# Kernel tuning notes

Hardware: AMD Instinct MI355X
Metric: run time of the kernel (lower is better)

The kernel has to match this reference:

```python
import jax, jax.numpy as jnp
import numpy as np

N_HIDDEN = 512

def _lstm_cell(x, h, c, W_ih, W_hh, b):
    # PyTorch LSTMCell: gates ordered i, f, g, o
    gates = x @ W_ih.T + h @ W_hh.T + b  # [B, 4H]
    i, f, g, o = jnp.split(gates, 4, axis=-1)
    i = jax.nn.sigmoid(i)
    f = jax.nn.sigmoid(f)
    g = jnp.tanh(g)
    o = jax.nn.sigmoid(o)
    c_new = f * c + i * g
    h_new = o * jnp.tanh(c_new)
    return h_new, c_new

def setup_inputs() -> dict:
    key = jax.random.key(0)
    ks = jax.random.split(key, 10)
    B, T, H = 256, 1024, N_HIDDEN
    s1 = 1.0 / np.sqrt(H)
    inp = {
        'x': jax.random.normal(ks[0], (B, T), dtype=jnp.float32),
        'W_ih1': jax.random.uniform(ks[1], (4 * H, 1), jnp.float32, -s1, s1),
        'W_hh1': jax.random.uniform(ks[2], (4 * H, H), jnp.float32, -s1, s1),
        'b1': jax.random.uniform(ks[3], (4 * H,), jnp.float32, -s1, s1),
        'W_ih2': jax.random.uniform(ks[4], (4 * H, H), jnp.float32, -s1, s1),
        'W_hh2': jax.random.uniform(ks[5], (4 * H, H), jnp.float32, -s1, s1),
        'b2': jax.random.uniform(ks[6], (4 * H,), jnp.float32, -s1, s1),
        'W_lin': jax.random.uniform(ks[7], (1, H), jnp.float32, -s1, s1),
        'b_lin': jax.random.uniform(ks[8], (1,), jnp.float32, -s1, s1),
    }
    return inp

def reference(x, W_ih1, W_hh1, b1, W_ih2, W_hh2, b2, W_lin, b_lin):
    B, T = x.shape
    H = W_hh1.shape[1]
    zeros = jnp.zeros((B, H), dtype=x.dtype)
    init = (zeros, zeros, zeros, zeros)
    xs = x.T[:, :, None]  # [T, B, 1]

    def step(carry, x_t):
        h1, c1, h2, c2 = carry
        h1, c1 = _lstm_cell(x_t, h1, c1, W_ih1, W_hh1, b1)
        h2, c2 = _lstm_cell(h1, h2, c2, W_ih2, W_hh2, b2)
        out = h2 @ W_lin.T + b_lin  # [B, 1]
        return (h1, c1, h2, c2), out

    _, outs = jax.lax.scan(step, init, xs)  # outs: [T, B, 1]
    return outs[:, :, 0].T  # [B, T]
```

## Files before the change

### kernel.cpp

```cpp
#include <hip/hip_runtime.h>
#include <math.h>

#define BB   256
#define TT   1024
#define HH   512
#define NWG  256
#define NTHR 512
#define SLOT (HH*BB)
#define NSLOT 8
#define PADX 20

typedef _Float16 f16;
typedef _Float16 f16x8 __attribute__((ext_vector_type(8)));
typedef float    f32x4 __attribute__((ext_vector_type(4)));
typedef unsigned int u32;
typedef u32 u32x2 __attribute__((ext_vector_type(2)));
typedef u32 u32x4 __attribute__((ext_vector_type(4)));
typedef unsigned short u16;
typedef unsigned char u8;

__device__ __forceinline__ f32x4 mf(f16x8 a, f16x8 b, f32x4 c){
  return __builtin_amdgcn_mfma_f32_16x16x32_f16(a, b, c, 0, 0, 0);
}

__device__ __forceinline__ float fast_sigmoid(float v){
  float e = __expf(-v);
  return __builtin_amdgcn_rcpf(1.0f + e);
}
__device__ __forceinline__ float fast_tanh(float v){
  float a = fabsf(v);
  float e = __expf(-2.0f * a);
  float r = (1.0f - e) * __builtin_amdgcn_rcpf(1.0f + e);
  return copysignf(r, v);
}

__device__ __forceinline__ void split_h(float hv, u16& hb, u8& lb){
  const f16 hh = (f16)hv;
  const f16 lh = (f16)((hv - (float)hh) * 2048.0f);
  union {f16 f; u16 u;} ch, cl; ch.f = hh; cl.f = lh;
  hb = ch.u;
  lb = (u8)(((u32)cl.u + 0x80u) >> 8);
}
__device__ __forceinline__ float join_h(u16 hb, u8 lb){
  union {u16 u; f16 f;} h, l;
  h.u = hb; l.u = (u16)((u32)lb << 8);
  return (float)h.f + (float)l.f * (1.0f/2048.0f);
}
__device__ __forceinline__ void st_wt_u16(u16* p, u16 v){
  __hip_atomic_store(p, v, __ATOMIC_RELAXED, __HIP_MEMORY_SCOPE_AGENT);
}
__device__ __forceinline__ void st_wt_u8(u8* p, u8 v){
  __hip_atomic_store(p, v, __ATOMIC_RELAXED, __HIP_MEMORY_SCOPE_AGENT);
}
__device__ __forceinline__ void st_wt_f32(float* p, float v){
  __hip_atomic_store(p, v, __ATOMIC_RELAXED, __HIP_MEMORY_SCOPE_AGENT);
}

__device__ __forceinline__ void build2(u32x4 hd, u32x2 ld2, f16x8& fh, f16x8& fl){
  union {u32 u[4]; f16x8 f;} H, L;
  H.u[0]=hd[0]; H.u[1]=hd[1]; H.u[2]=hd[2]; H.u[3]=hd[3];
  L.u[0] = __builtin_amdgcn_perm(ld2[0], 0u, 0x05010400u);
  L.u[1] = __builtin_amdgcn_perm(ld2[0], 0u, 0x07010600u);
  L.u[2] = __builtin_amdgcn_perm(ld2[1], 0u, 0x05010400u);
  L.u[3] = __builtin_amdgcn_perm(ld2[1], 0u, 0x07010600u);
  fh = H.f; fl = L.f;
}

struct St1 { u32x4 h4; u32x2 l2; };

__device__ __forceinline__ void gridbar_g(unsigned* barb, unsigned ph){
  __syncthreads();
  if (threadIdx.x == 0){
    __builtin_amdgcn_fence(__ATOMIC_RELEASE, "agent");
    const unsigned g = blockIdx.x & 31u;
    unsigned old = __hip_atomic_fetch_add(&barb[g*16], 1u, __ATOMIC_RELAXED, __HIP_MEMORY_SCOPE_AGENT);
    if (old + 1u == 8u*ph){
      unsigned om = __hip_atomic_fetch_add(&barb[512], 1u, __ATOMIC_RELAXED, __HIP_MEMORY_SCOPE_AGENT);
      if (om + 1u == 32u*ph){
        #pragma unroll
        for (int r = 0; r < 32; ++r)
          __hip_atomic_store(&barb[544 + r*16], ph, __ATOMIC_RELAXED, __HIP_MEMORY_SCOPE_AGENT);
      }
    }
    while (__hip_atomic_load(&barb[544 + g*16], __ATOMIC_RELAXED, __HIP_MEMORY_SCOPE_AGENT) < ph){
      __builtin_amdgcn_s_sleep(2);
    }
    __builtin_amdgcn_fence(__ATOMIC_ACQUIRE, "agent");
  }
  __syncthreads();
}

__global__ __launch_bounds__(NTHR, 2) void lstm_mfma(
    const float* __restrict__ x,      const float* __restrict__ W_ih1,
    const float* __restrict__ W_hh1,  const float* __restrict__ b1,
    const float* __restrict__ W_ih2,  const float* __restrict__ W_hh2,
    const float* __restrict__ b2,     const float* __restrict__ W_lin,
    const float* __restrict__ b_lin,  float* __restrict__ out,
    char* __restrict__ wsb)
{
  __shared__ f16x8 A2hi[2048], A2lo[2048], A1hi[1024], A1lo[1024];
  __shared__ float xch[8][16*PADX];
  __shared__ float wlin_s[512];
  __shared__ float outpart[2][8];

  unsigned* bar = (unsigned*)wsb;
  float* xT = (float*)(wsb + 16384);
  u16* h1h = (u16*)(wsb + 16384 + 1048576);
  u8*  h1l = (u8*) ((char*)h1h + 2*NSLOT*SLOT);
  u16* h2h = (u16*)((char*)h1l + NSLOT*SLOT);
  u8*  h2l = (u8*) ((char*)h2h + 2*NSLOT*SLOT);

  const int w   = blockIdx.x,  tid = threadIdx.x;
  const int l   = tid & 63,    wv  = tid >> 6;
  const int quad = l >> 4,     lc  = l & 15;
  const int p = w >> 1, cb = w & 1;
  const int j0 = 4*p;
  const int bcol = cb*128 + wv*16 + lc;
  const int jq = j0 + quad;
  const int b_out = cb*128 + p;
  unsigned* dbar = bar + cb*1024;
  unsigned* gbar = bar + 2048;
  const unsigned grp = (unsigned)(p >> 3);
  const int qrot = p & 3;
  const int hoff = (p>>1)*2048 + bcol*8 + (p&1)*4 + quad;

  {
    const int g_ = lc >> 2, jj_ = lc & 3;
    const int wrow = g_*HH + j0 + jj_;
    const float* rowI  = W_ih2 + (size_t)wrow*HH;
    const float* rowH2 = W_hh2 + (size_t)wrow*HH;
    const float* rowH1 = W_hh1 + (size_t)wrow*HH;
    for (int c = wv; c < 32; c += 8){
      const int kb = c*32 + quad*8;
      union {f16x8 v; f16 e[8];} hi8, lo8;
      #pragma unroll
      for (int i = 0; i < 8; ++i){
        const int k = kb + i;
        const float wval = (k < HH) ? rowI[k] : rowH2[k - HH];
        const f16 h_ = (f16)wval;
        hi8.e[i] = h_;
        lo8.e[i] = (f16)((wval - (float)h_) * 2048.0f);
      }
      A2hi[c*64 + l] = hi8.v;
      A2lo[c*64 + l] = lo8.v;
    }
    for (int c = wv; c < 16; c += 8){
      const int kb = c*32 + quad*8;
      union {f16x8 v; f16 e[8];} hi8, lo8;
      #pragma unroll
      for (int i = 0; i < 8; ++i){
        const float wval = rowH1[kb + i];
        const f16 h_ = (f16)wval;
        hi8.e[i] = h_;
        lo8.e[i] = (f16)((wval - (float)h_) * 2048.0f);
      }
      A1hi[c*64 + l] = hi8.v;
      A1lo[c*64 + l] = lo8.v;
    }
  }
  float wih1r[4], b1r[4], b2r[4];
  #pragma unroll
  for (int g = 0; g < 4; ++g){
    wih1r[g] = W_ih1[g*HH + jq];
    b1r[g]   = b1[g*HH + jq];
    b2r[g]   = b2[g*HH + jq];
  }
  const float blin = b_lin[0];
  wlin_s[tid] = W_lin[tid];

  {
    const int gid = w*NTHR + tid;
    #pragma unroll
    for (int i2 = 0; i2 < 2; ++i2){
      const int idx = gid + i2*131072;
      const int bb2 = idx >> 10, tt2 = idx & (TT-1);
      xT[(size_t)tt2*BB + bb2] = x[idx];
    }
  }
  {
    const int idx = w*NTHR + tid;
    st_wt_u16(&h2h[(NSLOT-1)*SLOT + idx], (u16)0);
    st_wt_u8 (&h2l[(NSLOT-1)*SLOT + idx], (u8)0);
  }

  gridbar_g(gbar, 1);

  float c1, c2 = 0.0f;
  {
    const float xv0 = xT[bcol];
    const float gi = fast_sigmoid(fmaf(xv0, wih1r[0], b1r[0]));
    const float gg = fast_tanh   (fmaf(xv0, wih1r[2], b1r[2]));
    const float go = fast_sigmoid(fmaf(xv0, wih1r[3], b1r[3]));
    c1 = gi * gg;
    const float hv = go * fast_tanh(c1);
    u16 hb; u8 lb; split_h(hv, hb, lb);
    st_wt_u16(&h1h[hoff], hb);
    st_wt_u8 (&h1l[hoff], lb);
  }
  gridbar_g(gbar, 2);

  auto poll2 = [&](unsigned need) -> unsigned {
    const int li = l & 31;
    const unsigned off = (unsigned)((li & 15) * 16) + ((li & 16) ? 576u : 0u);
    unsigned cv = __hip_atomic_load(&dbar[off], __ATOMIC_RELAXED, __HIP_MEMORY_SCOPE_AGENT);
    return (unsigned)__ballot(cv >= need);
  };

  unsigned got = 0xFFFFFFFFu;

  for (int t = 0; t < TT; ++t){
    const int sR1 = ( t            & (NSLOT-1))*SLOT;
    const int sR2 = ((t+NSLOT-1)   & (NSLOT-1))*SLOT;
    const int sW1 = ((t+1)         & (NSLOT-1))*SLOT;
    const int sW2 = ( t            & (NSLOT-1))*SLOT;
    const unsigned need = 8u * (unsigned)t;

    f32x4 aA2 = {0,0,0,0}, aB2 = {0,0,0,0}, aA1 = {0,0,0,0}, aB1 = {0,0,0,0};
    const u16* q1h = h1h + sR1 + quad*2048 + bcol*8;
    const u8*  q1l = h1l + sR1 + quad*2048 + bcol*8;
    const u16* q2h = h2h + sR2 + quad*2048 + bcol*8;
    const u8*  q2l = h2l + sR2 + quad*2048 + bcol*8;

    auto waitq = [&](int qq, int base){
      const unsigned qm = 0xFu << (base + 4*qq);
      while ((got & qm) != qm){
        __builtin_amdgcn_s_sleep(1);
        got |= poll2(need);
      }
      asm volatile("" ::: "memory");
    };
    auto ldc1 = [&](int c) -> St1 {
      St1 s; s.h4 = *(const u32x4*)(q1h + c*8192); s.l2 = *(const u32x2*)(q1l + c*8192); return s;
    };
    auto ldc2 = [&](int c) -> St1 {
      St1 s; s.h4 = *(const u32x4*)(q2h + c*8192); s.l2 = *(const u32x2*)(q2l + c*8192); return s;
    };
    auto cmp1 = [&](const St1& s, int c){
      f16x8 bh, bl;
      build2(s.h4, s.l2, bh, bl);
      const f16x8 a2h = A2hi[c*64 + l];
      const f16x8 a2l = A2lo[c*64 + l];
      const f16x8 a1h = A1hi[c*64 + l];
      const f16x8 a1l = A1lo[c*64 + l];
      aA2 = mf(a2h, bh, aA2);
      aB2 = mf(a2h, bl, aB2);
      aB2 = mf(a2l, bh, aB2);
      aA1 = mf(a1h, bh, aA1);
      aB1 = mf(a1h, bl, aB1);
      aB1 = mf(a1l, bh, aB1);
    };
    auto cmp2 = [&](const St1& s, int c){
      f16x8 ch, cl2;
      build2(s.h4, s.l2, ch, cl2);
      const f16x8 d2h = A2hi[(c+16)*64 + l];
      const f16x8 d2l = A2lo[(c+16)*64 + l];
      aA2 = mf(d2h, ch, aA2);
      aB2 = mf(d2h, cl2, aB2);
      aB2 = mf(d2l, ch, aB2);
    };

    const int cq0 = 4*qrot;
    const int cq1 = 4*((qrot+1)&3);
    const int cq2 = 4*((qrot+2)&3);
    const int cq3 = 4*((qrot+3)&3);

    {
      St1 SA0,SA1,SA2,SA3, SB0,SB1,SB2,SB3;
      waitq(cq0 >> 2, 16);
      SA0=ldc1(cq0+0); SA1=ldc1(cq0+1); SA2=ldc1(cq0+2); SA3=ldc1(cq0+3);
      waitq(cq1 >> 2, 16);
      SB0=ldc1(cq1+0); SB1=ldc1(cq1+1); SB2=ldc1(cq1+2); SB3=ldc1(cq1+3);
      cmp1(SA0,cq0+0); cmp1(SA1,cq0+1); cmp1(SA2,cq0+2); cmp1(SA3,cq0+3);
      waitq(cq2 >> 2, 16);
      SA0=ldc1(cq2+0); SA1=ldc1(cq2+1); SA2=ldc1(cq2+2); SA3=ldc1(cq2+3);
      cmp1(SB0,cq1+0); cmp1(SB1,cq1+1); cmp1(SB2,cq1+2); cmp1(SB3,cq1+3);
      waitq(cq3 >> 2, 16);
      SB0=ldc1(cq3+0); SB1=ldc1(cq3+1); SB2=ldc1(cq3+2); SB3=ldc1(cq3+3);
      cmp1(SA0,cq2+0); cmp1(SA1,cq2+1); cmp1(SA2,cq2+2); cmp1(SA3,cq2+3);
      cmp1(SB0,cq3+0); cmp1(SB1,cq3+1); cmp1(SB2,cq3+2); cmp1(SB3,cq3+3);
    }

    float* xw = &xch[wv][0];
    {
      f32x4 pre;
      #pragma unroll
      for (int i = 0; i < 4; ++i) pre[i] = fmaf(aB1[i], 1.0f/2048.0f, aA1[i]);
      __threadfence_block();
      *(f32x4*)&xw[lc*PADX + quad*4] = pre;
      __threadfence_block();
      const float g0 = xw[lc*PADX + 0*4 + quad];
      const float g1 = xw[lc*PADX + 1*4 + quad];
      const float g2 = xw[lc*PADX + 2*4 + quad];
      const float g3 = xw[lc*PADX + 3*4 + quad];
      const int tx = (t+1 < TT) ? (t+1) : (TT-1);
      const float xv = xT[(size_t)tx*BB + bcol];
      const float gi = fast_sigmoid(g0 + fmaf(xv, wih1r[0], b1r[0]));
      const float gf = fast_sigmoid(g1 + fmaf(xv, wih1r[1], b1r[1]));
      const float gg = fast_tanh   (g2 + fmaf(xv, wih1r[2], b1r[2]));
      const float go = fast_sigmoid(g3 + fmaf(xv, wih1r[3], b1r[3]));
      c1 = fmaf(gf, c1, gi*gg);
      const float hv = go * fast_tanh(c1);
      u16 hb; u8 lb; split_h(hv, hb, lb);
      st_wt_u16(&h1h[sW1 + hoff], hb);
      st_wt_u8 (&h1l[sW1 + hoff], lb);
    }
    __syncthreads();
    if (tid == 0){
      __builtin_amdgcn_fence(__ATOMIC_RELEASE, "workgroup");
      __hip_atomic_fetch_add(&dbar[576 + grp*16], 1u, __ATOMIC_RELAXED, __HIP_MEMORY_SCOPE_AGENT);
    }

    u16 ohb; u8 olb;
    {
      St1 SA0,SA1,SA2,SA3, SB0,SB1,SB2,SB3;
      waitq(cq0 >> 2, 0);
      SA0=ldc2(cq0+0); SA1=ldc2(cq0+1); SA2=ldc2(cq0+2); SA3=ldc2(cq0+3);
      waitq(cq1 >> 2, 0);
      SB0=ldc2(cq1+0); SB1=ldc2(cq1+1); SB2=ldc2(cq1+2); SB3=ldc2(cq1+3);
      cmp2(SA0,cq0+0); cmp2(SA1,cq0+1); cmp2(SA2,cq0+2); cmp2(SA3,cq0+3);
      waitq(cq2 >> 2, 0);
      SA0=ldc2(cq2+0); SA1=ldc2(cq2+1); SA2=ldc2(cq2+2); SA3=ldc2(cq2+3);
      cmp2(SB0,cq1+0); cmp2(SB1,cq1+1); cmp2(SB2,cq1+2); cmp2(SB3,cq1+3);
      waitq(cq3 >> 2, 0);
      SB0=ldc2(cq3+0); SB1=ldc2(cq3+1); SB2=ldc2(cq3+2); SB3=ldc2(cq3+3);
      const int oidx = sR2 + (tid>>3)*2048 + b_out*8 + (tid&7);
      ohb = h2h[oidx];
      olb = h2l[oidx];
      cmp2(SA0,cq2+0); cmp2(SA1,cq2+1); cmp2(SA2,cq2+2); cmp2(SA3,cq2+3);
      cmp2(SB0,cq3+0); cmp2(SB1,cq3+1); cmp2(SB2,cq3+2); cmp2(SB3,cq3+3);
    }

    float opart = join_h(ohb, olb) * wlin_s[tid];

    {
      f32x4 pre;
      #pragma unroll
      for (int i = 0; i < 4; ++i) pre[i] = fmaf(aB2[i], 1.0f/2048.0f, aA2[i]);
      __threadfence_block();
      *(f32x4*)&xw[lc*PADX + quad*4] = pre;
      __threadfence_block();
      const float g0 = xw[lc*PADX + 0*4 + quad];
      const float g1 = xw[lc*PADX + 1*4 + quad];
      const float g2 = xw[lc*PADX + 2*4 + quad];
      const float g3 = xw[lc*PADX + 3*4 + quad];
      const float gi = fast_sigmoid(g0 + b2r[0]);
      const float gf = fast_sigmoid(g1 + b2r[1]);
      const float gg = fast_tanh   (g2 + b2r[2]);
      const float go = fast_sigmoid(g3 + b2r[3]);
      c2 = fmaf(gf, c2, gi*gg);
      const float hv = go * fast_tanh(c2);
      u16 hb; u8 lb; split_h(hv, hb, lb);
      st_wt_u16(&h2h[sW2 + hoff], hb);
      st_wt_u8 (&h2l[sW2 + hoff], lb);
    }
    #pragma unroll
    for (int off = 32; off > 0; off >>= 1) opart += __shfl_down(opart, off, 64);
    if (l == 0) outpart[t & 1][wv] = opart;

    __syncthreads();
    if (tid == 0){
      __builtin_amdgcn_fence(__ATOMIC_RELEASE, "workgroup");
      __hip_atomic_fetch_add(&dbar[grp*16], 1u, __ATOMIC_RELAXED, __HIP_MEMORY_SCOPE_AGENT);
      if (t % 7 == 6){
        __builtin_amdgcn_fence(__ATOMIC_ACQUIRE, "agent");
      }
      if (t > 0){
        float s = blin;
        #pragma unroll
        for (int q2i = 0; q2i < 8; ++q2i) s += outpart[t & 1][q2i];
        st_wt_f32(&out[(size_t)b_out*TT + (t-1)], s);
      }
    }
    got = poll2(8u * (unsigned)(t+1));
    __syncthreads();
  }

  {
    const unsigned needT = 8u * (unsigned)TT;
    while ((got & 0xFFFFu) != 0xFFFFu){
      __builtin_amdgcn_s_sleep(1);
      got |= poll2(needT);
    }
    asm volatile("" ::: "memory");

    const int oidx = ((TT-1)&(NSLOT-1))*SLOT + (tid>>3)*2048 + b_out*8 + (tid&7);
    float opart = join_h(h2h[oidx], h2l[oidx]) * wlin_s[tid];
    #pragma unroll
    for (int off = 32; off > 0; off >>= 1) opart += __shfl_down(opart, off, 64);
    if (l == 0) outpart[0][wv] = opart;
    __syncthreads();
    if (tid == 0){
      float s = blin;
      #pragma unroll
      for (int q2i = 0; q2i < 8; ++q2i) s += outpart[0][q2i];
      st_wt_f32(&out[(size_t)b_out*TT + (TT-1)], s);
    }
  }
}

extern "C" void kernel_launch(void* const* d_in, const int* in_sizes, int n_in,
                              void* d_out, int out_size, void* d_ws, size_t ws_size,
                              hipStream_t stream) {
  const float* x     = (const float*)d_in[0];
  const float* W_ih1 = (const float*)d_in[1];
  const float* W_hh1 = (const float*)d_in[2];
  const float* b1    = (const float*)d_in[3];
  const float* W_ih2 = (const float*)d_in[4];
  const float* W_hh2 = (const float*)d_in[5];
  const float* b2    = (const float*)d_in[6];
  const float* W_lin = (const float*)d_in[7];
  const float* b_lin = (const float*)d_in[8];
  float* out = (float*)d_out;
  char* wsb  = (char*)d_ws;

  hipMemsetAsync(d_ws, 0, 16384, stream);

  hipLaunchKernelGGL(lstm_mfma, dim3(NWG), dim3(NTHR), 0, stream,
                     x, W_ih1, W_hh1, b1, W_ih2, W_hh2, b2, W_lin, b_lin, out, wsb);
}
```

Measured before the change: 13.03 ms.

## Move layer-2 input matmul after layer-1 publish and swap barrier roles

Layer-1's phase now computes only the W_hh1 product, issuing all 16 chunk loads before any MFMA. The W_ih2·h1 product moves into layer-2's phase, where both h1 and h2 chunks are loaded together. The two dbar counters swap roles so each phase waits on the right producer. The output reduction moves to a different thread and the trailing __syncthreads is dropped, aiming to publish h1 sooner and shorten the critical path between workgroups. The trade-offs are more register pressure from holding all 16 chunks, a heavier layer-2 phase, and subtle risks to ordering and correctness from the changed synchronisation.

```diff
diff --git a/kernel.cpp b/kernel.cpp
--- a/kernel.cpp
+++ b/kernel.cpp
@@ -66,6 +66,7 @@
   fh = H.f; fl = L.f;
 }
 
+struct St  { u32x4 h1h4; u32x2 h1l2; u32x4 h2h4; u32x2 h2l2; };
 struct St1 { u32x4 h4; u32x2 l2; };
 
 __device__ __forceinline__ void gridbar_g(unsigned* barb, unsigned ph){
@@ -215,7 +216,6 @@
     const int sW2 = ( t            & (NSLOT-1))*SLOT;
     const unsigned need = 8u * (unsigned)t;
 
-    f32x4 aA2 = {0,0,0,0}, aB2 = {0,0,0,0}, aA1 = {0,0,0,0}, aB1 = {0,0,0,0};
     const u16* q1h = h1h + sR1 + quad*2048 + bcol*8;
     const u8*  q1l = h1l + sR1 + quad*2048 + bcol*8;
     const u16* q2h = h2h + sR2 + quad*2048 + bcol*8;
@@ -229,55 +229,39 @@
       }
       asm volatile("" ::: "memory");
     };
-    auto ldc1 = [&](int c) -> St1 {
-      St1 s; s.h4 = *(const u32x4*)(q1h + c*8192); s.l2 = *(const u32x2*)(q1l + c*8192); return s;
-    };
-    auto ldc2 = [&](int c) -> St1 {
-      St1 s; s.h4 = *(const u32x4*)(q2h + c*8192); s.l2 = *(const u32x2*)(q2l + c*8192); return s;
-    };
-    auto cmp1 = [&](const St1& s, int c){
-      f16x8 bh, bl;
-      build2(s.h4, s.l2, bh, bl);
-      const f16x8 a2h = A2hi[c*64 + l];
-      const f16x8 a2l = A2lo[c*64 + l];
-      const f16x8 a1h = A1hi[c*64 + l];
-      const f16x8 a1l = A1lo[c*64 + l];
-      aA2 = mf(a2h, bh, aA2);
-      aB2 = mf(a2h, bl, aB2);
-      aB2 = mf(a2l, bh, aB2);
-      aA1 = mf(a1h, bh, aA1);
-      aB1 = mf(a1h, bl, aB1);
-      aB1 = mf(a1l, bh, aB1);
-    };
-    auto cmp2 = [&](const St1& s, int c){
-      f16x8 ch, cl2;
-      build2(s.h4, s.l2, ch, cl2);
-      const f16x8 d2h = A2hi[(c+16)*64 + l];
-      const f16x8 d2l = A2lo[(c+16)*64 + l];
-      aA2 = mf(d2h, ch, aA2);
-      aB2 = mf(d2h, cl2, aB2);
-      aB2 = mf(d2l, ch, aB2);
-    };
 
     const int cq0 = 4*qrot;
     const int cq1 = 4*((qrot+1)&3);
     const int cq2 = 4*((qrot+2)&3);
     const int cq3 = 4*((qrot+3)&3);
 
+    f32x4 aA1 = {0,0,0,0}, aB1 = {0,0,0,0};
     {
-      St1 SA0,SA1,SA2,SA3, SB0,SB1,SB2,SB3;
-      waitq(cq0 >> 2, 16);
-      SA0=ldc1(cq0+0); SA1=ldc1(cq0+1); SA2=ldc1(cq0+2); SA3=ldc1(cq0+3);
-      waitq(cq1 >> 2, 16);
-      SB0=ldc1(cq1+0); SB1=ldc1(cq1+1); SB2=ldc1(cq1+2); SB3=ldc1(cq1+3);
-      cmp1(SA0,cq0+0); cmp1(SA1,cq0+1); cmp1(SA2,cq0+2); cmp1(SA3,cq0+3);
-      waitq(cq2 >> 2, 16);
-      SA0=ldc1(cq2+0); SA1=ldc1(cq2+1); SA2=ldc1(cq2+2); SA3=ldc1(cq2+3);
-      cmp1(SB0,cq1+0); cmp1(SB1,cq1+1); cmp1(SB2,cq1+2); cmp1(SB3,cq1+3);
-      waitq(cq3 >> 2, 16);
-      SB0=ldc1(cq3+0); SB1=ldc1(cq3+1); SB2=ldc1(cq3+2); SB3=ldc1(cq3+3);
-      cmp1(SA0,cq2+0); cmp1(SA1,cq2+1); cmp1(SA2,cq2+2); cmp1(SA3,cq2+3);
-      cmp1(SB0,cq3+0); cmp1(SB1,cq3+1); cmp1(SB2,cq3+2); cmp1(SB3,cq3+3);
+      auto ld1 = [&](int c) -> St1 {
+        St1 s; s.h4 = *(const u32x4*)(q1h + c*8192); s.l2 = *(const u32x2*)(q1l + c*8192); return s;
+      };
+      auto cmp1 = [&](const St1& s, int c){
+        f16x8 bh, bl;
+        build2(s.h4, s.l2, bh, bl);
+        const f16x8 a1h = A1hi[c*64 + l];
+        const f16x8 a1l = A1lo[c*64 + l];
+        aA1 = mf(a1h, bh, aA1);
+        aB1 = mf(a1h, bl, aB1);
+        aB1 = mf(a1l, bh, aB1);
+      };
+      St1 P0,P1,P2,P3,P4,P5,P6,P7,P8,P9,P10,P11,P12,P13,P14,P15;
+      waitq(cq0 >> 2, 0);
+      P0=ld1(cq0+0); P1=ld1(cq0+1); P2=ld1(cq0+2); P3=ld1(cq0+3);
+      waitq(cq1 >> 2, 0);
+      P4=ld1(cq1+0); P5=ld1(cq1+1); P6=ld1(cq1+2); P7=ld1(cq1+3);
+      waitq(cq2 >> 2, 0);
+      P8=ld1(cq2+0); P9=ld1(cq2+1); P10=ld1(cq2+2); P11=ld1(cq2+3);
+      waitq(cq3 >> 2, 0);
+      P12=ld1(cq3+0); P13=ld1(cq3+1); P14=ld1(cq3+2); P15=ld1(cq3+3);
+      cmp1(P0,cq0+0); cmp1(P1,cq0+1); cmp1(P2,cq0+2); cmp1(P3,cq0+3);
+      cmp1(P4,cq1+0); cmp1(P5,cq1+1); cmp1(P6,cq1+2); cmp1(P7,cq1+3);
+      cmp1(P8,cq2+0); cmp1(P9,cq2+1); cmp1(P10,cq2+2); cmp1(P11,cq2+3);
+      cmp1(P12,cq3+0); cmp1(P13,cq3+1); cmp1(P14,cq3+2); cmp1(P15,cq3+3);
     }
 
     float* xw = &xch[wv][0];
@@ -307,27 +291,55 @@
     __syncthreads();
     if (tid == 0){
       __builtin_amdgcn_fence(__ATOMIC_RELEASE, "workgroup");
-      __hip_atomic_fetch_add(&dbar[576 + grp*16], 1u, __ATOMIC_RELAXED, __HIP_MEMORY_SCOPE_AGENT);
-    }
-
+      __hip_atomic_fetch_add(&dbar[grp*16], 1u, __ATOMIC_RELAXED, __HIP_MEMORY_SCOPE_AGENT);
+      if (t % 7 == 6){
+        __builtin_amdgcn_fence(__ATOMIC_ACQUIRE, "agent");
+      }
+    }
+
+    f32x4 aA2 = {0,0,0,0}, aB2 = {0,0,0,0};
     u16 ohb; u8 olb;
     {
-      St1 SA0,SA1,SA2,SA3, SB0,SB1,SB2,SB3;
-      waitq(cq0 >> 2, 0);
-      SA0=ldc2(cq0+0); SA1=ldc2(cq0+1); SA2=ldc2(cq0+2); SA3=ldc2(cq0+3);
-      waitq(cq1 >> 2, 0);
-      SB0=ldc2(cq1+0); SB1=ldc2(cq1+1); SB2=ldc2(cq1+2); SB3=ldc2(cq1+3);
-      cmp2(SA0,cq0+0); cmp2(SA1,cq0+1); cmp2(SA2,cq0+2); cmp2(SA3,cq0+3);
-      waitq(cq2 >> 2, 0);
-      SA0=ldc2(cq2+0); SA1=ldc2(cq2+1); SA2=ldc2(cq2+2); SA3=ldc2(cq2+3);
-      cmp2(SB0,cq1+0); cmp2(SB1,cq1+1); cmp2(SB2,cq1+2); cmp2(SB3,cq1+3);
-      waitq(cq3 >> 2, 0);
-      SB0=ldc2(cq3+0); SB1=ldc2(cq3+1); SB2=ldc2(cq3+2); SB3=ldc2(cq3+3);
+      auto ldc = [&](int c) -> St {
+        St s;
+        s.h1h4 = *(const u32x4*)(q1h + c*8192);
+        s.h1l2 = *(const u32x2*)(q1l + c*8192);
+        s.h2h4 = *(const u32x4*)(q2h + c*8192);
+        s.h2l2 = *(const u32x2*)(q2l + c*8192);
+        return s;
+      };
+      auto cmpP = [&](const St& s, int c){
+        f16x8 bh, bl;
+        build2(s.h1h4, s.h1l2, bh, bl);
+        const f16x8 a2h = A2hi[c*64 + l];
+        const f16x8 a2l = A2lo[c*64 + l];
+        aA2 = mf(a2h, bh, aA2);
+        aB2 = mf(a2h, bl, aB2);
+        aB2 = mf(a2l, bh, aB2);
+        f16x8 ch, cl2;
+        build2(s.h2h4, s.h2l2, ch, cl2);
+        const f16x8 d2h = A2hi[(c+16)*64 + l];
+        const f16x8 d2l = A2lo[(c+16)*64 + l];
+        aA2 = mf(d2h, ch, aA2);
+        aB2 = mf(d2h, cl2, aB2);
+        aB2 = mf(d2l, ch, aB2);
+      };
+      St SA0,SA1,SA2,SA3, SB0,SB1,SB2,SB3;
+      waitq(cq0 >> 2, 16);
+      SA0=ldc(cq0+0); SA1=ldc(cq0+1); SA2=ldc(cq0+2); SA3=ldc(cq0+3);
+      waitq(cq1 >> 2, 16);
+      SB0=ldc(cq1+0); SB1=ldc(cq1+1); SB2=ldc(cq1+2); SB3=ldc(cq1+3);
+      cmpP(SA0,cq0+0); cmpP(SA1,cq0+1); cmpP(SA2,cq0+2); cmpP(SA3,cq0+3);
+      waitq(cq2 >> 2, 16);
+      SA0=ldc(cq2+0); SA1=ldc(cq2+1); SA2=ldc(cq2+2); SA3=ldc(cq2+3);
+      cmpP(SB0,cq1+0); cmpP(SB1,cq1+1); cmpP(SB2,cq1+2); cmpP(SB3,cq1+3);
+      waitq(cq3 >> 2, 16);
+      SB0=ldc(cq3+0); SB1=ldc(cq3+1); SB2=ldc(cq3+2); SB3=ldc(cq3+3);
       const int oidx = sR2 + (tid>>3)*2048 + b_out*8 + (tid&7);
       ohb = h2h[oidx];
       olb = h2l[oidx];
-      cmp2(SA0,cq2+0); cmp2(SA1,cq2+1); cmp2(SA2,cq2+2); cmp2(SA3,cq2+3);
-      cmp2(SB0,cq3+0); cmp2(SB1,cq3+1); cmp2(SB2,cq3+2); cmp2(SB3,cq3+3);
+      cmpP(SA0,cq2+0); cmpP(SA1,cq2+1); cmpP(SA2,cq2+2); cmpP(SA3,cq2+3);
+      cmpP(SB0,cq3+0); cmpP(SB1,cq3+1); cmpP(SB2,cq3+2); cmpP(SB3,cq3+3);
     }
 
     float opart = join_h(ohb, olb) * wlin_s[tid];
@@ -360,24 +372,19 @@
     __syncthreads();
     if (tid == 0){
       __builtin_amdgcn_fence(__ATOMIC_RELEASE, "workgroup");
-      __hip_atomic_fetch_add(&dbar[grp*16], 1u, __ATOMIC_RELAXED, __HIP_MEMORY_SCOPE_AGENT);
-      if (t % 7 == 6){
-        __builtin_amdgcn_fence(__ATOMIC_ACQUIRE, "agent");
-      }
-      if (t > 0){
-        float s = blin;
-        #pragma unroll
-        for (int q2i = 0; q2i < 8; ++q2i) s += outpart[t & 1][q2i];
-        st_wt_f32(&out[(size_t)b_out*TT + (t-1)], s);
-      }
+      __hip_atomic_fetch_add(&dbar[576 + grp*16], 1u, __ATOMIC_RELAXED, __HIP_MEMORY_SCOPE_AGENT);
+    } else if (tid == 64 && t > 0){
+      float s = blin;
+      #pragma unroll
+      for (int q2i = 0; q2i < 8; ++q2i) s += outpart[t & 1][q2i];
+      st_wt_f32(&out[(size_t)b_out*TT + (t-1)], s);
     }
     got = poll2(8u * (unsigned)(t+1));
-    __syncthreads();
   }
 
   {
     const unsigned needT = 8u * (unsigned)TT;
-    while ((got & 0xFFFFu) != 0xFFFFu){
+    while (((got >> 16) & 0xFFFFu) != 0xFFFFu){
       __builtin_amdgcn_s_sleep(1);
       got |= poll2(needT);
     }
```

New measurement: 14.44 ms. 1.11x slower.
